# Performance work log

Measured on AMD Instinct MI355X. Metric: run time of the kernel, lower is better.

## Reference

```python
import jax, jax.numpy as jnp
import numpy as np

D_MODEL = 2048
NUM_HEADS = 16
D_K = D_MODEL // NUM_HEADS


def setup_inputs() -> dict:
    key = jax.random.key(0)
    ks = jax.random.split(key, 12)
    B, S, D = 2, 2048, D_MODEL
    s = 1.0 / np.sqrt(D)
    return {
        "q": jax.random.normal(ks[0], (B, S, D), jnp.float32),
        "k": jax.random.normal(ks[1], (B, S, D), jnp.float32),
        "v": jax.random.normal(ks[2], (B, S, D), jnp.float32),
        "Wq": jax.random.normal(ks[3], (D, D), jnp.float32) * s,
        "bq": jax.random.normal(ks[4], (D,), jnp.float32) * 0.01,
        "Wk": jax.random.normal(ks[5], (D, D), jnp.float32) * s,
        "bk": jax.random.normal(ks[6], (D,), jnp.float32) * 0.01,
        "Wv": jax.random.normal(ks[7], (D, D), jnp.float32) * s,
        "bv": jax.random.normal(ks[8], (D,), jnp.float32) * 0.01,
        "Wo": jax.random.normal(ks[9], (D, D), jnp.float32) * s,
        "bo": jax.random.normal(ks[10], (D,), jnp.float32) * 0.01,
    }


def reference(q, k, v, Wq, bq, Wk, bk, Wv, bv, Wo, bo):
    B, S, D = q.shape
    H, dk = NUM_HEADS, D_K

    def proj(x, W, b):
        # Linear then split heads -> [B, H, S, dk]
        y = jnp.einsum('bsd,df->bsf', x, W) + b
        return y.reshape(B, -1, H, dk).transpose(0, 2, 1, 3)

    Q = proj(q, Wq, bq)
    K = proj(k, Wk, bk)
    V = proj(v, Wv, bv)

    scores = jnp.einsum('bhqd,bhkd->bhqk', Q, K) / jnp.sqrt(jnp.float32(dk))
    attn = jax.nn.softmax(scores, axis=-1)  # dropout is identity (eval)
    out = jnp.einsum('bhqk,bhkd->bhqd', attn, V)
    out = out.transpose(0, 2, 1, 3).reshape(B, -1, D)
    return jnp.einsum('bsd,df->bsf', out, Wo) + bo
```

## Files before the change

kernel.cpp:

```cpp
#include <hip/hip_runtime.h>
#include <hip/hip_bf16.h>
#include <stdint.h>

typedef float  f32x4  __attribute__((ext_vector_type(4)));
typedef float  f32x16 __attribute__((ext_vector_type(16)));
typedef short  s16x8  __attribute__((ext_vector_type(8)));

#define D_MODEL 2048
#define NHEADS  16
#define DK      128
#define BATCH   2
#define SEQ     2048
#define MROWS   (BATCH*SEQ)

__device__ __forceinline__ unsigned short f2bf(float f) {
  union { float f; unsigned int u; } v; v.f = f;
  unsigned int r = v.u + 0x7FFFu + ((v.u >> 16) & 1u);
  return (unsigned short)(r >> 16);
}

__device__ __forceinline__ unsigned int packbf_c(float lo, float hi) {
  __hip_bfloat16 l = __float2bfloat16(lo);
  __hip_bfloat16 h = __float2bfloat16(hi);
  unsigned short lu, hu;
  __builtin_memcpy(&lu, &l, 2);
  __builtin_memcpy(&hu, &h, 2);
  return (unsigned int)lu | ((unsigned int)hu << 16);
}

__device__ __forceinline__ void async16(const void* g, void* l) {
  __builtin_amdgcn_global_load_lds(
      (const __attribute__((address_space(1))) unsigned int*)g,
      (__attribute__((address_space(3))) unsigned int*)l,
      16, 0, 0);
}

__global__ __launch_bounds__(256) void f2b3_kernel(const float* __restrict__ q,
                                                   const float* __restrict__ k,
                                                   const float* __restrict__ v,
                                                   unsigned short* __restrict__ qb,
                                                   unsigned short* __restrict__ kb,
                                                   unsigned short* __restrict__ vb) {
  const float* s; unsigned short* d;
  switch (blockIdx.y) {
    case 0:  s = q; d = qb; break;
    case 1:  s = k; d = kb; break;
    default: s = v; d = vb; break;
  }
  int i = blockIdx.x * 256 + threadIdx.x;
  const float4* s4 = (const float4*)s;
  float4 a = s4[2*i];
  float4 b = s4[2*i+1];
  s16x8 o;
  o[0] = (short)f2bf(a.x); o[1] = (short)f2bf(a.y);
  o[2] = (short)f2bf(a.z); o[3] = (short)f2bf(a.w);
  o[4] = (short)f2bf(b.x); o[5] = (short)f2bf(b.y);
  o[6] = (short)f2bf(b.z); o[7] = (short)f2bf(b.w);
  *(s16x8*)(d + 8*(size_t)i) = o;
}

__global__ __launch_bounds__(256) void wtrans_kernel(const float* __restrict__ Wq,
                                                     const float* __restrict__ Wk,
                                                     const float* __restrict__ Wv,
                                                     const float* __restrict__ Wo,
                                                     unsigned short* __restrict__ WqT,
                                                     unsigned short* __restrict__ WkT,
                                                     unsigned short* __restrict__ WvT,
                                                     unsigned short* __restrict__ WoT) {
  const float* W; unsigned short* Wt;
  switch (blockIdx.z) {
    case 0:  W = Wq; Wt = WqT; break;
    case 1:  W = Wk; Wt = WkT; break;
    case 2:  W = Wv; Wt = WvT; break;
    default: W = Wo; Wt = WoT; break;
  }
  __shared__ float tl[32][33];
  int x = threadIdx.x, y = threadIdx.y;
  int n0 = blockIdx.x * 32, k0 = blockIdx.y * 32;
  #pragma unroll
  for (int j = 0; j < 32; j += 8)
    tl[y + j][x] = W[(size_t)(k0 + y + j) * D_MODEL + n0 + x];
  __syncthreads();
  #pragma unroll
  for (int j = 0; j < 32; j += 8)
    Wt[(size_t)(n0 + y + j) * D_MODEL + k0 + x] = f2bf(tl[x][y + j]);
}

__device__ __forceinline__ void gemm256_core(const unsigned short* __restrict__ A,
                                             const unsigned short* __restrict__ Bt,
                                             const float* __restrict__ bias,
                                             void* __restrict__ Cout,
                                             int N, int K, int mode, float scale,
                                             int m0, int n0, unsigned short* lds) {
  const int t  = threadIdx.x;
  const int l  = t & 63, w = t >> 6;
  const int wm = w >> 2, wn = w & 3;
  const int lr = l & 15, lg = l >> 4;

  unsigned short* Ab[2] = { lds,         lds + 24576 };
  unsigned short* Bb[2] = { lds + 8192,  lds + 24576 + 8192 };

  auto STAGE = [&](int buf, int kt) {
    unsigned short* Ad = Ab[buf];
    unsigned short* Bd = Bb[buf];
    #pragma unroll
    for (int i = 0; i < 2; ++i) {
      int c = t + 512*i;
      int row = c >> 3, crs = (c & 7) ^ (row & 7);
      async16(A + (size_t)(m0 + row)*K + kt*64 + crs*8, (char*)Ad + c*16);
    }
    #pragma unroll
    for (int i = 0; i < 4; ++i) {
      int c = t + 512*i;
      int row = c >> 3, crs = (c & 7) ^ (row & 7);
      async16(Bt + (size_t)(n0 + row)*K + kt*64 + crs*8, (char*)Bd + c*16);
    }
  };

  const int NT = K >> 6;
  STAGE(0, 0);
  __syncthreads();

  f32x4 acc[4][4] = {};

  for (int kt = 0; kt < NT; ++kt) {
    const int cur = kt & 1;
    if (kt + 1 < NT) STAGE(cur ^ 1, kt + 1);
    const unsigned short* Ac = Ab[cur];
    const unsigned short* Bc = Bb[cur];

    #pragma unroll
    for (int ks = 0; ks < 2; ++ks) {
      const int cb = ks*64 + lg*16;
      s16x8 af[4], bf[4];
      #pragma unroll
      for (int mf = 0; mf < 4; ++mf) {
        int row = wm*64 + mf*16 + lr;
        af[mf] = *(const s16x8*)((const char*)Ac + row*128 + (cb ^ ((row & 7) << 4)));
      }
      #pragma unroll
      for (int nf = 0; nf < 4; ++nf) {
        int row = wn*64 + nf*16 + lr;
        bf[nf] = *(const s16x8*)((const char*)Bc + row*128 + (cb ^ ((row & 7) << 4)));
      }
      __builtin_amdgcn_s_setprio(1);
      #pragma unroll
      for (int mf = 0; mf < 4; ++mf)
        #pragma unroll
        for (int nf = 0; nf < 4; ++nf)
          acc[mf][nf] = __builtin_amdgcn_mfma_f32_16x16x32_bf16(af[mf], bf[nf], acc[mf][nf], 0, 0, 0);
      __builtin_amdgcn_s_setprio(0);
    }

    __syncthreads();
  }

  if (mode == 0) {
    float* C = (float*)Cout;
    #pragma unroll
    for (int nf = 0; nf < 4; ++nf) {
      int col = n0 + wn*64 + nf*16 + lr;
      float bv = bias[col];
      #pragma unroll
      for (int mf = 0; mf < 4; ++mf) {
        int rowb = m0 + wm*64 + mf*16 + lg*4;
        #pragma unroll
        for (int r = 0; r < 4; ++r)
          C[(size_t)(rowb + r)*N + col] = (acc[mf][nf][r] + bv) * scale;
      }
    }
  } else {
    unsigned short* C = (unsigned short*)Cout;
    #pragma unroll
    for (int nf = 0; nf < 4; ++nf) {
      int col = n0 + wn*64 + nf*16 + lr;
      float bv = bias[col];
      int h = col >> 7, dkk = col & 127;
      #pragma unroll
      for (int mf = 0; mf < 4; ++mf) {
        int rowb = m0 + wm*64 + mf*16 + lg*4;
        #pragma unroll
        for (int r = 0; r < 4; ++r) {
          int row = rowb + r;
          int b = row >> 11, s = row & 2047;
          C[((size_t)((b*NHEADS + h)*SEQ + s))*DK + dkk] = f2bf((acc[mf][nf][r] + bv) * scale);
        }
      }
    }
  }
}

__global__ __launch_bounds__(512) void gemm256_qkv(const unsigned short* __restrict__ qb,
                                                   const unsigned short* __restrict__ kb,
                                                   const unsigned short* __restrict__ vb,
                                                   const unsigned short* __restrict__ WT,
                                                   const float* __restrict__ bq,
                                                   const float* __restrict__ bk,
                                                   const float* __restrict__ bv,
                                                   unsigned short* __restrict__ Hout,
                                                   float qscale) {
  __shared__ unsigned short lds[49152];
  const int z = blockIdx.z;
  const unsigned short* A = (z == 0) ? qb : (z == 1) ? kb : vb;
  const float* bias       = (z == 0) ? bq : (z == 1) ? bk : bv;
  const float scale       = (z == 0) ? qscale : 1.0f;
  const unsigned short* Bt = WT + (size_t)z * D_MODEL * D_MODEL;
  unsigned short* Cout     = Hout + (size_t)z * MROWS * D_MODEL;
  gemm256_core(A, Bt, bias, Cout, D_MODEL, D_MODEL, 1, scale,
               blockIdx.y*128, blockIdx.x*256, lds);
}

__global__ __launch_bounds__(512) void gemm256_out(const unsigned short* __restrict__ A,
                                                   const unsigned short* __restrict__ Bt,
                                                   const float* __restrict__ bias,
                                                   float* __restrict__ Cout) {
  __shared__ unsigned short lds[49152];
  gemm256_core(A, Bt, bias, Cout, D_MODEL, D_MODEL, 0, 1.0f,
               blockIdx.y*128, blockIdx.x*256, lds);
}

__global__ __launch_bounds__(256, 2) void attn_kernel(const unsigned short* __restrict__ Q,
                                                      const unsigned short* __restrict__ K,
                                                      const unsigned short* __restrict__ V,
                                                      unsigned short* __restrict__ O) {
  __shared__ char lds[64*256 + 128*144];
  unsigned short* Kl = (unsigned short*)lds;
  unsigned short* Vt = (unsigned short*)(lds + 64*256);

  const int t  = threadIdx.x;
  const int l  = t & 63, w = t >> 6;
  const int q_ = l & 31, hi = l >> 5;
  const int bh = blockIdx.y;
  const int b  = bh >> 4, h = bh & 15;
  const int q0 = blockIdx.x * 128;

  const unsigned short* Qp = Q + (size_t)bh * SEQ * DK;
  const unsigned short* Kp = K + (size_t)bh * SEQ * DK;
  const unsigned short* Vp = V + (size_t)bh * SEQ * DK;

  const int qrow = q0 + w*32 + q_;
  s16x8 aq[8];
  #pragma unroll
  for (int kk = 0; kk < 8; ++kk)
    aq[kk] = *(const s16x8*)(Qp + (size_t)qrow*DK + kk*16 + hi*8);

  f32x16 accO[4] = {};
  float m = -INFINITY, L = 0.f;

  const int vp_ = t & 31;
  const int vd0 = (t >> 5) * 8;

  const int NT = SEQ/64;
  s16x8 va0, vb0, va1, vb1;

  va0 = *(const s16x8*)(Vp + (size_t)(2*vp_    )*DK + vd0);
  vb0 = *(const s16x8*)(Vp + (size_t)(2*vp_ + 1)*DK + vd0);
  va1 = *(const s16x8*)(Vp + (size_t)(2*vp_    )*DK + vd0 + 64);
  vb1 = *(const s16x8*)(Vp + (size_t)(2*vp_ + 1)*DK + vd0 + 64);
  #pragma unroll
  for (int i = 0; i < 4; ++i) {
    int c   = t + 256*i;
    int row = c >> 4;
    int sb  = ((c & 15) << 4) ^ ((row & 15) << 4);
    async16((const char*)(Kp + (size_t)row*DK) + sb, (char*)Kl + c*16);
  }
  asm volatile("" ::: "memory");

  for (int tt = 0; tt < NT; ++tt) {
    asm volatile("s_waitcnt vmcnt(4)" ::: "memory");
    #pragma unroll
    for (int j = 0; j < 8; ++j) {
      unsigned int pk0 = (unsigned int)(unsigned short)va0[j]
                       | ((unsigned int)(unsigned short)vb0[j] << 16);
      *(unsigned int*)&Vt[(vd0 + j)*72 + 2*vp_] = pk0;
      unsigned int pk1 = (unsigned int)(unsigned short)va1[j]
                       | ((unsigned int)(unsigned short)vb1[j] << 16);
      *(unsigned int*)&Vt[(vd0 + 64 + j)*72 + 2*vp_] = pk1;
    }
    __syncthreads();

    f32x16 S0 = {}, S1 = {};
    #pragma unroll
    for (int t2 = 0; t2 < 2; ++t2) {
      int krow = t2*32 + q_;
      const char* kb = (const char*)Kl + krow*256;
      int swz = (krow & 15) << 4;
      #pragma unroll
      for (int kk = 0; kk < 8; ++kk) {
        s16x8 kf = *(const s16x8*)(kb + ((kk*32 + hi*16) ^ swz));
        if (t2 == 0) S0 = __builtin_amdgcn_mfma_f32_32x32x16_bf16(kf, aq[kk], S0, 0, 0, 0);
        else         S1 = __builtin_amdgcn_mfma_f32_32x32x16_bf16(kf, aq[kk], S1, 0, 0, 0);
      }
    }
    __syncthreads();

    if (tt + 1 < NT) {
      int kvn = (tt + 1) * 64;
      va0 = *(const s16x8*)(Vp + (size_t)(kvn + 2*vp_    )*DK + vd0);
      vb0 = *(const s16x8*)(Vp + (size_t)(kvn + 2*vp_ + 1)*DK + vd0);
      va1 = *(const s16x8*)(Vp + (size_t)(kvn + 2*vp_    )*DK + vd0 + 64);
      vb1 = *(const s16x8*)(Vp + (size_t)(kvn + 2*vp_ + 1)*DK + vd0 + 64);
      #pragma unroll
      for (int i = 0; i < 4; ++i) {
        int c   = t + 256*i;
        int row = c >> 4;
        int sb  = ((c & 15) << 4) ^ ((row & 15) << 4);
        async16((const char*)(Kp + (size_t)(kvn + row)*DK) + sb, (char*)Kl + c*16);
      }
      asm volatile("" ::: "memory");
    }

    f32x16 mx;
    #pragma unroll
    for (int r = 0; r < 16; ++r) mx[r] = fmaxf(S0[r], S1[r]);
    float m8_[8];
    #pragma unroll
    for (int r = 0; r < 8; ++r) m8_[r] = fmaxf(mx[r], mx[r+8]);
    float m4a = fmaxf(m8_[0], m8_[4]), m4b = fmaxf(m8_[1], m8_[5]);
    float m4c = fmaxf(m8_[2], m8_[6]), m4d = fmaxf(m8_[3], m8_[7]);
    float pmax = fmaxf(fmaxf(m4a, m4b), fmaxf(m4c, m4d));
    pmax = fmaxf(pmax, __shfl_xor(pmax, 32, 64));

    if (!__all(pmax <= m + 11.0f)) {
      float mnew = fmaxf(m, pmax);
      float corr = exp2f(m - mnew);
      m = mnew;
      L *= corr;
      #pragma unroll
      for (int sub = 0; sub < 4; ++sub)
        #pragma unroll
        for (int r = 0; r < 16; ++r) accO[sub][r] *= corr;
    }

    float rs0 = 0.f, rs1 = 0.f, rs2 = 0.f, rs3 = 0.f;
    #pragma unroll
    for (int r = 0; r < 4; ++r) {
      float a0 = exp2f(S0[r]    - m); S0[r]    = a0; rs0 += a0;
      float a1 = exp2f(S0[r+4]  - m); S0[r+4]  = a1; rs1 += a1;
      float a2 = exp2f(S0[r+8]  - m); S0[r+8]  = a2; rs2 += a2;
      float a3 = exp2f(S0[r+12] - m); S0[r+12] = a3; rs3 += a3;
      float b0 = exp2f(S1[r]    - m); S1[r]    = b0; rs0 += b0;
      float b1 = exp2f(S1[r+4]  - m); S1[r+4]  = b1; rs1 += b1;
      float b2 = exp2f(S1[r+8]  - m); S1[r+8]  = b2; rs2 += b2;
      float b3 = exp2f(S1[r+12] - m); S1[r+12] = b3; rs3 += b3;
    }
    float rs = (rs0 + rs1) + (rs2 + rs3);
    rs += __shfl_xor(rs, 32, 64);
    L += rs;

    s16x8 PB[4];
    #pragma unroll
    for (int t2 = 0; t2 < 2; ++t2) {
      #pragma unroll
      for (int half = 0; half < 2; ++half) {
        int bse = half*8;
        unsigned int pkA01, pkA23, pkB01, pkB23;
        if (t2 == 0) {
          pkA01 = packbf_c(S0[bse+0], S0[bse+1]);
          pkA23 = packbf_c(S0[bse+2], S0[bse+3]);
          pkB01 = packbf_c(S0[bse+4], S0[bse+5]);
          pkB23 = packbf_c(S0[bse+6], S0[bse+7]);
        } else {
          pkA01 = packbf_c(S1[bse+0], S1[bse+1]);
          pkA23 = packbf_c(S1[bse+2], S1[bse+3]);
          pkB01 = packbf_c(S1[bse+4], S1[bse+5]);
          pkB23 = packbf_c(S1[bse+6], S1[bse+7]);
        }
        unsigned int xA01 = __shfl_xor(pkA01, 32, 64);
        unsigned int xA23 = __shfl_xor(pkA23, 32, 64);
        unsigned int xB01 = __shfl_xor(pkB01, 32, 64);
        unsigned int xB23 = __shfl_xor(pkB23, 32, 64);
        union { unsigned int u[4]; s16x8 v; } f;
        f.u[0] = hi ? xB01 : pkA01;
        f.u[1] = hi ? xB23 : pkA23;
        f.u[2] = hi ? pkB01 : xA01;
        f.u[3] = hi ? pkB23 : xA23;
        PB[t2*2 + half] = f.v;
      }
    }

    #pragma unroll
    for (int sub = 0; sub < 4; ++sub) {
      const char* vb2 = (const char*)Vt + (size_t)(sub*32 + q_)*144 + hi*16;
      #pragma unroll
      for (int kk = 0; kk < 4; ++kk) {
        s16x8 vf = *(const s16x8*)(vb2 + kk*32);
        accO[sub] = __builtin_amdgcn_mfma_f32_32x32x16_bf16(vf, PB[kk], accO[sub], 0, 0, 0);
      }
    }

    __builtin_amdgcn_s_barrier();
  }

  __syncthreads();
  unsigned short* Ob = (unsigned short*)lds + (size_t)w*4096;
  float inv = 1.0f / L;
  #pragma unroll
  for (int sub = 0; sub < 4; ++sub)
    #pragma unroll
    for (int j = 0; j < 8; ++j) {
      unsigned int pw = packbf_c(accO[sub][2*j]*inv, accO[sub][2*j+1]*inv);
      int dv = sub*32 + (j&1)*2 + ((j>>1)*8) + 4*hi;
      *(unsigned int*)((char*)Ob + q_*256 + ((dv*2) ^ ((q_ & 15) << 4))) = pw;
    }
  asm volatile("s_waitcnt lgkmcnt(0)" ::: "memory");
  size_t gbase = ((size_t)(b*SEQ + q0 + w*32 + q_))*D_MODEL + h*DK;
  #pragma unroll
  for (int p = 0; p < 8; ++p) {
    int chunk = hi + 2*p;
    s16x8 ov = *(const s16x8*)((char*)Ob + q_*256 + ((chunk*16) ^ ((q_ & 15) << 4)));
    *(s16x8*)(O + gbase + chunk*8) = ov;
  }
}

extern "C" void kernel_launch(void* const* d_in, const int* in_sizes, int n_in,
                              void* d_out, int out_size, void* d_ws, size_t ws_size,
                              hipStream_t stream) {
  const float* q  = (const float*)d_in[0];
  const float* k  = (const float*)d_in[1];
  const float* v  = (const float*)d_in[2];
  const float* Wq = (const float*)d_in[3];
  const float* bq = (const float*)d_in[4];
  const float* Wk = (const float*)d_in[5];
  const float* bk = (const float*)d_in[6];
  const float* Wv = (const float*)d_in[7];
  const float* bv = (const float*)d_in[8];
  const float* Wo = (const float*)d_in[9];
  const float* bo = (const float*)d_in[10];
  float* out = (float*)d_out;

  char* ws = (char*)d_ws;
  const size_t SZT = (size_t)MROWS * D_MODEL * 2;
  const size_t SZW = (size_t)D_MODEL * D_MODEL * 2;

  unsigned short* qb  = (unsigned short*)(ws);
  unsigned short* kb  = (unsigned short*)(ws + SZT);
  unsigned short* vb  = (unsigned short*)(ws + 2*SZT);
  unsigned short* WqT = (unsigned short*)(ws + 3*SZT);
  unsigned short* WkT = (unsigned short*)(ws + 3*SZT + SZW);
  unsigned short* WvT = (unsigned short*)(ws + 3*SZT + 2*SZW);
  unsigned short* WoT = (unsigned short*)(ws + 3*SZT + 3*SZW);
  unsigned short* Qh  = (unsigned short*)(ws + 3*SZT + 4*SZW);
  unsigned short* Kh  = (unsigned short*)(ws + 4*SZT + 4*SZW);
  unsigned short* Vh  = (unsigned short*)(ws + 5*SZT + 4*SZW);
  unsigned short* Oc  = qb;

  const int n8 = MROWS * D_MODEL / 8;
  f2b3_kernel<<<dim3(n8/256, 3), 256, 0, stream>>>(q, k, v, qb, kb, vb);
  wtrans_kernel<<<dim3(64, 64, 4), dim3(32, 8), 0, stream>>>(Wq, Wk, Wv, Wo, WqT, WkT, WvT, WoT);

  const float qscale = 0.1275174308f;
  gemm256_qkv<<<dim3(D_MODEL/256, MROWS/128, 3), 512, 0, stream>>>(qb, kb, vb, WqT, bq, bk, bv, Qh, qscale);

  attn_kernel<<<dim3(SEQ/128, BATCH*NHEADS), 256, 0, stream>>>(Qh, Kh, Vh, Oc);

  gemm256_out<<<dim3(D_MODEL/256, MROWS/128), 512, 0, stream>>>(Oc, WoT, bo, out);
}
```

Before: 363.4 us.

## Enlarge GEMM tiles to 256x256 with interleaved prefetch and block swizzle

The shared GEMM core now computes a 256x256 output tile per 512-thread block instead of 128x256, using 128KB of double-buffered LDS and 8x4 accumulator fragments per wave. The global-to-LDS prefetch of the next K tile is split into A and B halves and issued between the MFMA groups, with explicit barriers and waitcnts replacing the single end-of-iteration sync. Block indices are remapped with a swizzle to improve L2 reuse. The goal is higher arithmetic intensity per loaded byte. The cost is halving the block count: the output projection drops to 128 blocks and QKV to 384, which can leave CUs idle or create a tail wave.

```diff
diff --git a/kernel.cpp b/kernel.cpp
--- a/kernel.cpp
+++ b/kernel.cpp
@@ -91,68 +91,86 @@
                                              const float* __restrict__ bias,
                                              void* __restrict__ Cout,
                                              int N, int K, int mode, float scale,
-                                             int m0, int n0, unsigned short* lds) {
+                                             int m0, int n0, char* lds) {
   const int t  = threadIdx.x;
   const int l  = t & 63, w = t >> 6;
   const int wm = w >> 2, wn = w & 3;
   const int lr = l & 15, lg = l >> 4;
 
-  unsigned short* Ab[2] = { lds,         lds + 24576 };
-  unsigned short* Bb[2] = { lds + 8192,  lds + 24576 + 8192 };
-
-  auto STAGE = [&](int buf, int kt) {
-    unsigned short* Ad = Ab[buf];
-    unsigned short* Bd = Bb[buf];
-    #pragma unroll
-    for (int i = 0; i < 2; ++i) {
-      int c = t + 512*i;
-      int row = c >> 3, crs = (c & 7) ^ (row & 7);
-      async16(A + (size_t)(m0 + row)*K + kt*64 + crs*8, (char*)Ad + c*16);
-    }
+  char* Abuf[2] = { lds,          lds + 65536 };
+  char* Bbuf[2] = { lds + 32768,  lds + 65536 + 32768 };
+
+  auto stageA = [&](int buf, int kt) {
     #pragma unroll
     for (int i = 0; i < 4; ++i) {
       int c = t + 512*i;
-      int row = c >> 3, crs = (c & 7) ^ (row & 7);
-      async16(Bt + (size_t)(n0 + row)*K + kt*64 + crs*8, (char*)Bd + c*16);
+      int row = c >> 3;
+      int crs = (c & 7) ^ (row & 7);
+      async16(A + (size_t)(m0 + row)*K + kt*64 + crs*8, Abuf[buf] + c*16);
     }
   };
+  auto stageB = [&](int buf, int kt) {
+    #pragma unroll
+    for (int i = 0; i < 4; ++i) {
+      int c = t + 512*i;
+      int row = c >> 3;
+      int crs = (c & 7) ^ (row & 7);
+      async16(Bt + (size_t)(n0 + row)*K + kt*64 + crs*8, Bbuf[buf] + c*16);
+    }
+  };
 
   const int NT = K >> 6;
-  STAGE(0, 0);
-  __syncthreads();
-
-  f32x4 acc[4][4] = {};
+  stageA(0, 0); stageB(0, 0);
+  asm volatile("s_waitcnt vmcnt(0)" ::: "memory");
+  __builtin_amdgcn_s_barrier();
+
+  f32x4 acc[8][4] = {};
 
   for (int kt = 0; kt < NT; ++kt) {
     const int cur = kt & 1;
-    if (kt + 1 < NT) STAGE(cur ^ 1, kt + 1);
-    const unsigned short* Ac = Ab[cur];
-    const unsigned short* Bc = Bb[cur];
+    const char* Ac = Abuf[cur];
+    const char* Bc = Bbuf[cur];
+    const bool pre = (kt + 1 < NT);
 
     #pragma unroll
     for (int ks = 0; ks < 2; ++ks) {
       const int cb = ks*64 + lg*16;
-      s16x8 af[4], bf[4];
-      #pragma unroll
-      for (int mf = 0; mf < 4; ++mf) {
-        int row = wm*64 + mf*16 + lr;
-        af[mf] = *(const s16x8*)((const char*)Ac + row*128 + (cb ^ ((row & 7) << 4)));
-      }
+      s16x8 bf[4];
       #pragma unroll
       for (int nf = 0; nf < 4; ++nf) {
         int row = wn*64 + nf*16 + lr;
-        bf[nf] = *(const s16x8*)((const char*)Bc + row*128 + (cb ^ ((row & 7) << 4)));
-      }
-      __builtin_amdgcn_s_setprio(1);
-      #pragma unroll
-      for (int mf = 0; mf < 4; ++mf)
+        bf[nf] = *(const s16x8*)(Bc + row*128 + (cb ^ ((row & 7) << 4)));
+      }
+      #pragma unroll
+      for (int mh = 0; mh < 2; ++mh) {
+        s16x8 af[4];
         #pragma unroll
-        for (int nf = 0; nf < 4; ++nf)
-          acc[mf][nf] = __builtin_amdgcn_mfma_f32_16x16x32_bf16(af[mf], bf[nf], acc[mf][nf], 0, 0, 0);
-      __builtin_amdgcn_s_setprio(0);
-    }
-
-    __syncthreads();
+        for (int mf = 0; mf < 4; ++mf) {
+          int row = wm*128 + (mh*4 + mf)*16 + lr;
+          af[mf] = *(const s16x8*)(Ac + row*128 + (cb ^ ((row & 7) << 4)));
+        }
+        if (ks == 0 && pre) {
+          if (mh == 0) stageA(cur ^ 1, kt + 1);
+          else         stageB(cur ^ 1, kt + 1);
+        }
+        __builtin_amdgcn_s_barrier();
+        asm volatile("s_waitcnt lgkmcnt(0)" ::: "memory");
+        __builtin_amdgcn_sched_barrier(0);
+        __builtin_amdgcn_s_setprio(1);
+        #pragma unroll
+        for (int mf = 0; mf < 4; ++mf)
+          #pragma unroll
+          for (int nf = 0; nf < 4; ++nf)
+            acc[mh*4 + mf][nf] = __builtin_amdgcn_mfma_f32_16x16x32_bf16(af[mf], bf[nf],
+                                                                         acc[mh*4 + mf][nf], 0, 0, 0);
+        __builtin_amdgcn_s_setprio(0);
+        __builtin_amdgcn_s_barrier();
+      }
+    }
+    if (pre) {
+      asm volatile("s_waitcnt vmcnt(0)" ::: "memory");
+      __builtin_amdgcn_s_barrier();
+    }
   }
 
   if (mode == 0) {
@@ -162,11 +180,11 @@
       int col = n0 + wn*64 + nf*16 + lr;
       float bv = bias[col];
       #pragma unroll
-      for (int mf = 0; mf < 4; ++mf) {
-        int rowb = m0 + wm*64 + mf*16 + lg*4;
+      for (int m8 = 0; m8 < 8; ++m8) {
+        int rowb = m0 + wm*128 + m8*16 + lg*4;
         #pragma unroll
         for (int r = 0; r < 4; ++r)
-          C[(size_t)(rowb + r)*N + col] = (acc[mf][nf][r] + bv) * scale;
+          C[(size_t)(rowb + r)*N + col] = (acc[m8][nf][r] + bv) * scale;
       }
     }
   } else {
@@ -177,17 +195,24 @@
       float bv = bias[col];
       int h = col >> 7, dkk = col & 127;
       #pragma unroll
-      for (int mf = 0; mf < 4; ++mf) {
-        int rowb = m0 + wm*64 + mf*16 + lg*4;
+      for (int m8 = 0; m8 < 8; ++m8) {
+        int rowb = m0 + wm*128 + m8*16 + lg*4;
         #pragma unroll
         for (int r = 0; r < 4; ++r) {
           int row = rowb + r;
           int b = row >> 11, s = row & 2047;
-          C[((size_t)((b*NHEADS + h)*SEQ + s))*DK + dkk] = f2bf((acc[mf][nf][r] + bv) * scale);
+          C[((size_t)((b*NHEADS + h)*SEQ + s))*DK + dkk] = f2bf((acc[m8][nf][r] + bv) * scale);
         }
       }
     }
   }
+}
+
+__device__ __forceinline__ void swz_mn(int& m0, int& n0) {
+  int lin = blockIdx.x + 8*blockIdx.y;
+  int swz = (lin & 7)*16 + (lin >> 3);
+  n0 = (swz >> 4) * 256;
+  m0 = (swz & 15) * 256;
 }
 
 __global__ __launch_bounds__(512) void gemm256_qkv(const unsigned short* __restrict__ qb,
@@ -199,24 +224,24 @@
                                                    const float* __restrict__ bv,
                                                    unsigned short* __restrict__ Hout,
                                                    float qscale) {
-  __shared__ unsigned short lds[49152];
+  __shared__ char lds[131072];
   const int z = blockIdx.z;
   const unsigned short* A = (z == 0) ? qb : (z == 1) ? kb : vb;
   const float* bias       = (z == 0) ? bq : (z == 1) ? bk : bv;
   const float scale       = (z == 0) ? qscale : 1.0f;
   const unsigned short* Bt = WT + (size_t)z * D_MODEL * D_MODEL;
   unsigned short* Cout     = Hout + (size_t)z * MROWS * D_MODEL;
-  gemm256_core(A, Bt, bias, Cout, D_MODEL, D_MODEL, 1, scale,
-               blockIdx.y*128, blockIdx.x*256, lds);
+  int m0, n0; swz_mn(m0, n0);
+  gemm256_core(A, Bt, bias, Cout, D_MODEL, D_MODEL, 1, scale, m0, n0, lds);
 }
 
 __global__ __launch_bounds__(512) void gemm256_out(const unsigned short* __restrict__ A,
                                                    const unsigned short* __restrict__ Bt,
                                                    const float* __restrict__ bias,
                                                    float* __restrict__ Cout) {
-  __shared__ unsigned short lds[49152];
-  gemm256_core(A, Bt, bias, Cout, D_MODEL, D_MODEL, 0, 1.0f,
-               blockIdx.y*128, blockIdx.x*256, lds);
+  __shared__ char lds[131072];
+  int m0, n0; swz_mn(m0, n0);
+  gemm256_core(A, Bt, bias, Cout, D_MODEL, D_MODEL, 0, 1.0f, m0, n0, lds);
 }
 
 __global__ __launch_bounds__(256, 2) void attn_kernel(const unsigned short* __restrict__ Q,
@@ -450,9 +475,9 @@
   wtrans_kernel<<<dim3(64, 64, 4), dim3(32, 8), 0, stream>>>(Wq, Wk, Wv, Wo, WqT, WkT, WvT, WoT);
 
   const float qscale = 0.1275174308f;
-  gemm256_qkv<<<dim3(D_MODEL/256, MROWS/128, 3), 512, 0, stream>>>(qb, kb, vb, WqT, bq, bk, bv, Qh, qscale);
+  gemm256_qkv<<<dim3(8, 16, 3), 512, 0, stream>>>(qb, kb, vb, WqT, bq, bk, bv, Qh, qscale);
 
   attn_kernel<<<dim3(SEQ/128, BATCH*NHEADS), 256, 0, stream>>>(Qh, Kh, Vh, Oc);
 
-  gemm256_out<<<dim3(D_MODEL/256, MROWS/128), 512, 0, stream>>>(Oc, WoT, bo, out);
-}
+  gemm256_out<<<dim3(8, 16), 512, 0, stream>>>(Oc, WoT, bo, out);
+}
```

After: 469.2 us. 29.1% more time.
